# Optimization experiments

Hardware: AMD Instinct MI355X
Metric: run time of the kernel (lower is better)

## Reference

```python
import jax, jax.numpy as jnp
import numpy as np

B, T, C = 4, 2048, 1024
H = 16
D = C // H  # head_dim = 64


def setup_inputs() -> dict:
    key = jax.random.key(0)
    ks = jax.random.split(key, 9)
    s = 1.0 / np.sqrt(C)
    return {
        "x": jax.random.normal(ks[0], (B, T, C), dtype=jnp.float32),
        "Wq": jax.random.normal(ks[1], (C, C), dtype=jnp.float32) * s,
        "bq": jnp.zeros((C,), dtype=jnp.float32),
        "Wk": jax.random.normal(ks[2], (C, C), dtype=jnp.float32) * s,
        "bk": jnp.zeros((C,), dtype=jnp.float32),
        "Wv": jax.random.normal(ks[3], (C, C), dtype=jnp.float32) * s,
        "bv": jnp.zeros((C,), dtype=jnp.float32),
        "Wp": jax.random.normal(ks[4], (C, C), dtype=jnp.float32) * s,
        "bp": jnp.zeros((C,), dtype=jnp.float32),
    }


def reference(x, Wq, bq, Wk, bk, Wv, bv, Wp, bp):
    # Linear projections; reshape to [B, H, T, D]
    def split_heads(y):
        return y.reshape(B, T, H, D).transpose(0, 2, 1, 3)

    q = split_heads(x @ Wq + bq)
    k = split_heads(x @ Wk + bk)
    v = split_heads(x @ Wv + bv)

    scale = 1.0 / np.sqrt(D)
    att = jnp.einsum('bhqd,bhkd->bhqk', q, k) * scale  # [B,H,T,T]
    att = jax.nn.softmax(att, axis=-1)
    # dropout with p=0.0 is identity
    out = jnp.einsum('bhqk,bhkd->bhqd', att, v)        # [B,H,T,D]
    out = out.transpose(0, 2, 1, 3).reshape(B, T, C)
    return out @ Wp + bp
```

## Files before the change

kernel.cpp:

```cpp
#include <hip/hip_runtime.h>


#define B_ 4
#define T_ 2048
#define C_ 1024
#define H_ 16
#define D_ 64

#define QSCALE 0.18033688011112042f

typedef float  f32x4  __attribute__((ext_vector_type(4)));
typedef __bf16 bf16x8 __attribute__((ext_vector_type(8)));
typedef __bf16 bf16x4 __attribute__((ext_vector_type(4)));
typedef __bf16 bf16x2 __attribute__((ext_vector_type(2)));
typedef unsigned uint2v __attribute__((ext_vector_type(2)));

typedef const __attribute__((address_space(1))) void gv_t;
typedef __attribute__((address_space(3))) void lds_t;

__device__ __forceinline__ void async_load16(const void* g, void* l) {
  __builtin_amdgcn_global_load_lds((gv_t*)g, (lds_t*)l, 16, 0, 0);
}

__device__ __forceinline__ float fast_exp2(float x) {
#if __has_builtin(__builtin_amdgcn_exp2f)
  return __builtin_amdgcn_exp2f(x);
#else
  return exp2f(x);
#endif
}

__device__ __forceinline__ void pl16_swap(unsigned& a, unsigned& b) {
#if __has_builtin(__builtin_amdgcn_permlane16_swap)
  uint2v r = __builtin_amdgcn_permlane16_swap(a, b, false, false);
  a = r[0];
  b = r[1];
#else
  asm("v_permlane16_swap_b32 %0, %1" : "+v"(a), "+v"(b));
#endif
}

__global__ __launch_bounds__(256) void cast_f32_bf16(
    const float* __restrict__ in, __bf16* __restrict__ out, int n) {
  int i = (blockIdx.x * 256 + threadIdx.x) * 8;
  if (i >= n) return;
  float4 a = *(const float4*)(in + i);
  float4 b = *(const float4*)(in + i + 4);
  bf16x8 o;
  o[0] = (__bf16)a.x; o[1] = (__bf16)a.y; o[2] = (__bf16)a.z; o[3] = (__bf16)a.w;
  o[4] = (__bf16)b.x; o[5] = (__bf16)b.y; o[6] = (__bf16)b.z; o[7] = (__bf16)b.w;
  *(bf16x8*)(out + i) = o;
}

__global__ __launch_bounds__(256) void transpose_cast_w(
    const float* __restrict__ W0, const float* __restrict__ W1,
    const float* __restrict__ W2, const float* __restrict__ W3,
    __bf16* __restrict__ out) {
  int z = blockIdx.z;
  const float* W = (z == 0) ? W0 : (z == 1) ? W1 : (z == 2) ? W2 : W3;
  __bf16* o = out + (size_t)z * (C_ * C_);
  __shared__ __align__(16) __bf16 sT[64][72];
  int tid = threadIdx.x;
  int n0 = blockIdx.x * 64, k0 = blockIdx.y * 64;
#pragma unroll
  for (int i = 0; i < 4; i++) {
    int s = tid + i * 256;
    int kr = s >> 4, nc = (s & 15) * 4;
    float4 v = *(const float4*)&W[(size_t)(k0 + kr) * C_ + n0 + nc];
    bf16x4 t;
    t[0] = (__bf16)v.x; t[1] = (__bf16)v.y; t[2] = (__bf16)v.z; t[3] = (__bf16)v.w;
    *(bf16x4*)&sT[kr][nc] = t;
  }
  __syncthreads();
#pragma unroll
  for (int i = 0; i < 2; i++) {
    int s = tid + i * 256;
    int nr = s >> 3, kc = (s & 7) * 8;
    bf16x8 ov;
#pragma unroll
    for (int j = 0; j < 8; j++) ov[j] = sT[kc + j][nr];
    *(bf16x8*)&o[(size_t)(n0 + nr) * C_ + k0 + kc] = ov;
  }
}

template <typename OutT, int EPI>
__device__ __forceinline__ void gemm_body(
    const __bf16* __restrict__ A, const __bf16* __restrict__ Bt,
    const float* __restrict__ bias, OutT* __restrict__ C, int N, int K,
    float scale, int m0, int n0) {
  __shared__ __align__(16) __bf16 sA[128 * 32];
  __shared__ __align__(16) __bf16 sB[128 * 32];
  int tid = threadIdx.x, lane = tid & 63, wave = tid >> 6;
  int lr = lane & 15, quad = lane >> 4;
  int wm = (wave & 1) * 64, wn = (wave >> 1) * 64;

  const f32x4 zero = {0.f, 0.f, 0.f, 0.f};
  f32x4 acc[4][4];
#pragma unroll
  for (int i = 0; i < 4; i++)
#pragma unroll
    for (int j = 0; j < 4; j++) acc[i][j] = zero;

  for (int k0 = 0; k0 < K; k0 += 32) {
    __syncthreads();
#pragma unroll
    for (int i = 0; i < 2; i++) {
      int s = tid + i * 256;
      int r = s >> 2, c8 = (s & 3) * 8;
      async_load16(A + (size_t)(m0 + r) * K + k0 + c8, &sA[s * 8]);
      async_load16(Bt + (size_t)(n0 + r) * K + k0 + c8, &sB[s * 8]);
    }
    __syncthreads();
    bf16x8 af[4], bfr[4];
#pragma unroll
    for (int mt = 0; mt < 4; mt++)
      af[mt] = *(const bf16x8*)&sA[(wm + mt * 16 + lr) * 32 + quad * 8];
#pragma unroll
    for (int nt = 0; nt < 4; nt++)
      bfr[nt] = *(const bf16x8*)&sB[(wn + nt * 16 + lr) * 32 + quad * 8];
#pragma unroll
    for (int mt = 0; mt < 4; mt++)
#pragma unroll
      for (int nt = 0; nt < 4; nt++)
        acc[mt][nt] = __builtin_amdgcn_mfma_f32_16x16x32_bf16(
            af[mt], bfr[nt], acc[mt][nt], 0, 0, 0);
  }
  if (EPI == 0) {
#pragma unroll
    for (int mt = 0; mt < 4; mt++) {
#pragma unroll
      for (int nt = 0; nt < 4; nt++) {
        int n = n0 + wn + nt * 16 + lr;
        float bv = bias[n];
#pragma unroll
        for (int r = 0; r < 4; r++) {
          int m = m0 + wm + mt * 16 + quad * 4 + r;
          C[(size_t)m * N + n] = (OutT)((acc[mt][nt][r] + bv) * scale);
        }
      }
    }
  } else {
    int bb = m0 >> 11;
    int mloc0 = (m0 & (T_ - 1)) + wm;
    __bf16* Ct = (__bf16*)C;
#pragma unroll
    for (int mt = 0; mt < 4; mt++) {
      int pos = ((quad & 1) << 5) | ((((quad >> 1) << 1) | (mt & 1)) << 3) |
                ((mt >> 1) << 2);
#pragma unroll
      for (int nt = 0; nt < 4; nt++) {
        int n = n0 + wn + nt * 16 + lr;
        float bv = bias[n];
        bf16x4 ov;
#pragma unroll
        for (int r = 0; r < 4; r++) ov[r] = (__bf16)(acc[mt][nt][r] + bv);
        *(bf16x4*)&Ct[((size_t)bb * C_ + n) * T_ + mloc0 + pos] = ov;
      }
    }
  }
}

__global__ __launch_bounds__(256) void gemm_qkv_kernel(
    const __bf16* __restrict__ A, const __bf16* __restrict__ WT,
    const float* __restrict__ b0, const float* __restrict__ b1,
    const float* __restrict__ b2, __bf16* __restrict__ qkbase,
    __bf16* __restrict__ Vt) {
  int l = blockIdx.x;
  int xcd = l & 7;
  int idx = l >> 3;
  int z = idx >> 6;
  int rem = idx & 63;
  int m0 = (xcd * 8 + (rem >> 3)) * 128;
  int n0 = (rem & 7) * 128;
  if (z == 2) {
    gemm_body<__bf16, 1>(A, WT + (size_t)2 * C_ * C_, b2, Vt, C_, C_, 1.0f,
                         m0, n0);
  } else {
    const float* bias = (z == 0) ? b0 : b1;
    float scale = (z == 0) ? QSCALE : 1.0f;
    gemm_body<__bf16, 0>(A, WT + (size_t)z * C_ * C_, bias,
                         qkbase + (size_t)z * (B_ * T_) * C_, C_, C_, scale,
                         m0, n0);
  }
}

__global__ __launch_bounds__(256) void gemm_proj_kernel(
    const __bf16* __restrict__ A, const __bf16* __restrict__ Bt,
    const float* __restrict__ bias, float* __restrict__ C) {
  int l = blockIdx.x;
  int xcd = l & 7;
  int idx = l >> 3;
  int m0 = (xcd * 8 + (idx >> 3)) * 128;
  int n0 = (idx & 7) * 128;
  gemm_body<float, 0>(A, Bt, bias, C, C_, C_, 1.0f, m0, n0);
}

__global__ __launch_bounds__(256) void attn_kernel(
    const __bf16* __restrict__ Q, const __bf16* __restrict__ K,
    const __bf16* __restrict__ Vt, __bf16* __restrict__ O) {
  __shared__ __align__(16) __bf16 sK[64 * 72];
  __shared__ __align__(16) __bf16 sV[64 * 72];
  int tid = threadIdx.x, wave = tid >> 6, lane = tid & 63;
  int lr = lane & 15, quad = lane >> 4;
  int l = blockIdx.x;
  int bh = (l & 7) * 8 + ((l >> 3) & 7);
  int xbq = l >> 6;
  int b = bh >> 4, h = bh & 15;
  int qw = xbq * 256 + wave * 64;

  bf16x8 aq[4][2];
#pragma unroll
  for (int s = 0; s < 4; s++) {
    const __bf16* qp =
        Q + ((size_t)(b * T_ + qw + s * 16 + lr)) * C_ + h * D_ + quad * 8;
    aq[s][0] = *(const bf16x8*)qp;
    aq[s][1] = *(const bf16x8*)(qp + 32);
  }

  bf16x8 onesf;
#pragma unroll
  for (int j = 0; j < 8; j++) onesf[j] = (__bf16)1.0f;

  const f32x4 zero = {0.f, 0.f, 0.f, 0.f};
  f32x4 accO[4][4];
  f32x4 accL[4] = {zero, zero, zero, zero};
#pragma unroll
  for (int s = 0; s < 4; s++)
#pragma unroll
    for (int d = 0; d < 4; d++) accO[s][d] = zero;

  int srow[2], sc8[2];
#pragma unroll
  for (int i = 0; i < 2; i++) {
    int s = tid + i * 256;
    srow[i] = s >> 3;
    sc8[i] = (s & 7) * 8;
  }

  bf16x8 kreg[2], vreg[2];
#pragma unroll
  for (int i = 0; i < 2; i++) {
    kreg[i] = *(const bf16x8*)(K + ((size_t)(b * T_ + srow[i])) * C_ + h * D_ + sc8[i]);
    vreg[i] = *(const bf16x8*)(Vt + ((size_t)(bh * D_ + srow[i])) * T_ + sc8[i]);
  }

  for (int k0 = 0; k0 < T_; k0 += 64) {
    __builtin_amdgcn_sched_barrier(0);
    __builtin_amdgcn_s_barrier();
    __builtin_amdgcn_sched_barrier(0);
#pragma unroll
    for (int i = 0; i < 2; i++) {
      *(bf16x8*)&sK[srow[i] * 72 + sc8[i]] = kreg[i];
      *(bf16x8*)&sV[srow[i] * 72 + sc8[i]] = vreg[i];
    }
    __builtin_amdgcn_sched_barrier(0);
    asm volatile("s_waitcnt lgkmcnt(0)" ::: "memory");
    __builtin_amdgcn_s_barrier();
    __builtin_amdgcn_sched_barrier(0);

    if (k0 + 64 < T_) {
      int kn = k0 + 64;
#pragma unroll
      for (int i = 0; i < 2; i++) {
        kreg[i] = *(const bf16x8*)(K + ((size_t)(b * T_ + kn + srow[i])) * C_ + h * D_ + sc8[i]);
        vreg[i] = *(const bf16x8*)(Vt + ((size_t)(bh * D_ + srow[i])) * T_ + kn + sc8[i]);
      }
    }

    bf16x8 bkf[4][2];
#pragma unroll
    for (int nt = 0; nt < 4; nt++) {
      bkf[nt][0] = *(const bf16x8*)&sK[(nt * 16 + lr) * 72 + quad * 8];
      bkf[nt][1] = *(const bf16x8*)&sK[(nt * 16 + lr) * 72 + 32 + quad * 8];
    }

    bf16x8 bpA[4], bpB[4];
#pragma unroll
    for (int s = 0; s < 4; s++) {
      unsigned pw[4][2];
#pragma unroll
      for (int nt = 0; nt < 4; nt++) {
        f32x4 z = zero;
        z = __builtin_amdgcn_mfma_f32_16x16x32_bf16(bkf[nt][0], aq[s][0], z, 0, 0, 0);
        z = __builtin_amdgcn_mfma_f32_16x16x32_bf16(bkf[nt][1], aq[s][1], z, 0, 0, 0);
        union { bf16x2 h; unsigned u; } t0, t1;
        t0.h[0] = (__bf16)fast_exp2(z[0]);
        t0.h[1] = (__bf16)fast_exp2(z[1]);
        t1.h[0] = (__bf16)fast_exp2(z[2]);
        t1.h[1] = (__bf16)fast_exp2(z[3]);
        pw[nt][0] = t0.u;
        pw[nt][1] = t1.u;
      }
      unsigned a0 = pw[0][0], b0 = pw[1][0]; pl16_swap(a0, b0);
      unsigned a1 = pw[0][1], b1 = pw[1][1]; pl16_swap(a1, b1);
      unsigned a2 = pw[2][0], b2 = pw[3][0]; pl16_swap(a2, b2);
      unsigned a3 = pw[2][1], b3 = pw[3][1]; pl16_swap(a3, b3);
      union { unsigned u[4]; bf16x8 v; } pA, pB;
      pA.u[0] = a0; pA.u[1] = a1; pA.u[2] = a2; pA.u[3] = a3;
      pB.u[0] = b0; pB.u[1] = b1; pB.u[2] = b2; pB.u[3] = b3;
      bpA[s] = pA.v;
      bpB[s] = pB.v;
      accL[s] = __builtin_amdgcn_mfma_f32_16x16x32_bf16(onesf, bpA[s], accL[s], 0, 0, 0);
      accL[s] = __builtin_amdgcn_mfma_f32_16x16x32_bf16(onesf, bpB[s], accL[s], 0, 0, 0);
    }
#pragma unroll
    for (int dt = 0; dt < 4; dt++) {
      bf16x8 av0 = *(const bf16x8*)&sV[(dt * 16 + lr) * 72 + quad * 8];
      bf16x8 av1 = *(const bf16x8*)&sV[(dt * 16 + lr) * 72 + 32 + quad * 8];
#pragma unroll
      for (int s = 0; s < 4; s++) {
        accO[s][dt] = __builtin_amdgcn_mfma_f32_16x16x32_bf16(av0, bpA[s], accO[s][dt], 0, 0, 0);
        accO[s][dt] = __builtin_amdgcn_mfma_f32_16x16x32_bf16(av1, bpB[s], accO[s][dt], 0, 0, 0);
      }
    }
  }

#pragma unroll
  for (int s = 0; s < 4; s++) {
    float inv = 1.0f / accL[s][0];
    __bf16* op =
        O + ((size_t)(b * T_ + qw + s * 16 + lr)) * C_ + h * D_ + quad * 4;
#pragma unroll
    for (int dt = 0; dt < 4; dt++) {
      bf16x4 ov;
#pragma unroll
      for (int r = 0; r < 4; r++) ov[r] = (__bf16)(accO[s][dt][r] * inv);
      *(bf16x4*)&op[dt * 16] = ov;
    }
  }
}

extern "C" void kernel_launch(void* const* d_in, const int* in_sizes, int n_in,
                              void* d_out, int out_size, void* d_ws, size_t ws_size,
                              hipStream_t stream) {
  const float* x  = (const float*)d_in[0];
  const float* Wq = (const float*)d_in[1];
  const float* bq = (const float*)d_in[2];
  const float* Wk = (const float*)d_in[3];
  const float* bk = (const float*)d_in[4];
  const float* Wv = (const float*)d_in[5];
  const float* bv = (const float*)d_in[6];
  const float* Wp = (const float*)d_in[7];
  const float* bp = (const float*)d_in[8];
  float* out = (float*)d_out;

  char* ws = (char*)d_ws;
  const size_t MB = 1024 * 1024;
  __bf16* xb    = (__bf16*)(ws + 0 * MB);
  __bf16* WT    = (__bf16*)(ws + 16 * MB);
  __bf16* Qb    = (__bf16*)(ws + 24 * MB);
  __bf16* Kb    = Qb + (size_t)(B_ * T_) * C_;
  __bf16* Vt    = Kb + (size_t)(B_ * T_) * C_;
  __bf16* attnb = (__bf16*)(ws + 72 * MB);
  __bf16* WpT   = WT + (size_t)3 * C_ * C_;

  cast_f32_bf16<<<dim3(4096), dim3(256), 0, stream>>>(x, xb, B_ * T_ * C_);
  transpose_cast_w<<<dim3(16, 16, 4), dim3(256), 0, stream>>>(Wq, Wk, Wv, Wp, WT);
  gemm_qkv_kernel<<<dim3(1536), dim3(256), 0, stream>>>(xb, WT, bq, bk, bv, Qb, Vt);
  attn_kernel<<<dim3(512), dim3(256), 0, stream>>>(Qb, Kb, Vt, attnb);
  gemm_proj_kernel<<<dim3(512), dim3(256), 0, stream>>>(attnb, WpT, bp, out);
}
```

Baseline: 268.2 us.

## Merge prep kernels, halve proj GEMM N-tile, raise priority on PV MFMAs

Merges the x cast and the weight transpose-cast into one launch to save a kernel launch and overlap the two prep jobs. Templates the GEMM on the N tile width and runs the output projection with 128x64 tiles, doubling its grid to 1024 blocks so it fills the CUs better (256 CUs on MI355X). Adds s_setprio around the P·V MFMA block in attention to favour matrix issue across waves. The trade-off is more redundant A-tile loads in the projection GEMM.

New measurement: 267.5 us. Within noise of the previous version (-0.3%).

```diff
diff --git a/kernel.cpp b/kernel.cpp
--- a/kernel.cpp
+++ b/kernel.cpp
@@ -40,36 +40,38 @@
 #endif
 }
 
-__global__ __launch_bounds__(256) void cast_f32_bf16(
-    const float* __restrict__ in, __bf16* __restrict__ out, int n) {
-  int i = (blockIdx.x * 256 + threadIdx.x) * 8;
-  if (i >= n) return;
-  float4 a = *(const float4*)(in + i);
-  float4 b = *(const float4*)(in + i + 4);
-  bf16x8 o;
-  o[0] = (__bf16)a.x; o[1] = (__bf16)a.y; o[2] = (__bf16)a.z; o[3] = (__bf16)a.w;
-  o[4] = (__bf16)b.x; o[5] = (__bf16)b.y; o[6] = (__bf16)b.z; o[7] = (__bf16)b.w;
-  *(bf16x8*)(out + i) = o;
-}
-
-__global__ __launch_bounds__(256) void transpose_cast_w(
+__global__ __launch_bounds__(256) void prep_kernel(
+    const float* __restrict__ x, __bf16* __restrict__ xb,
     const float* __restrict__ W0, const float* __restrict__ W1,
     const float* __restrict__ W2, const float* __restrict__ W3,
-    __bf16* __restrict__ out) {
-  int z = blockIdx.z;
+    __bf16* __restrict__ wt) {
+  __shared__ __align__(16) __bf16 sT[64][72];
+  int l = blockIdx.x;
+  int tid = threadIdx.x;
+  if (l < 4096) {
+    int i = (l * 256 + tid) * 8;
+    float4 a = *(const float4*)(x + i);
+    float4 b = *(const float4*)(x + i + 4);
+    bf16x8 o;
+    o[0] = (__bf16)a.x; o[1] = (__bf16)a.y; o[2] = (__bf16)a.z; o[3] = (__bf16)a.w;
+    o[4] = (__bf16)b.x; o[5] = (__bf16)b.y; o[6] = (__bf16)b.z; o[7] = (__bf16)b.w;
+    *(bf16x8*)(xb + i) = o;
+    return;
+  }
+  int t = l - 4096;
+  int z = t >> 8;
+  int k0 = ((t >> 4) & 15) * 64;
+  int n0 = (t & 15) * 64;
   const float* W = (z == 0) ? W0 : (z == 1) ? W1 : (z == 2) ? W2 : W3;
-  __bf16* o = out + (size_t)z * (C_ * C_);
-  __shared__ __align__(16) __bf16 sT[64][72];
-  int tid = threadIdx.x;
-  int n0 = blockIdx.x * 64, k0 = blockIdx.y * 64;
+  __bf16* o = wt + (size_t)z * (C_ * C_);
 #pragma unroll
   for (int i = 0; i < 4; i++) {
     int s = tid + i * 256;
     int kr = s >> 4, nc = (s & 15) * 4;
     float4 v = *(const float4*)&W[(size_t)(k0 + kr) * C_ + n0 + nc];
-    bf16x4 t;
-    t[0] = (__bf16)v.x; t[1] = (__bf16)v.y; t[2] = (__bf16)v.z; t[3] = (__bf16)v.w;
-    *(bf16x4*)&sT[kr][nc] = t;
+    bf16x4 tt;
+    tt[0] = (__bf16)v.x; tt[1] = (__bf16)v.y; tt[2] = (__bf16)v.z; tt[3] = (__bf16)v.w;
+    *(bf16x4*)&sT[kr][nc] = tt;
   }
   __syncthreads();
 #pragma unroll
@@ -83,23 +85,25 @@
   }
 }
 
-template <typename OutT, int EPI>
+template <typename OutT, int EPI, int BN>
 __device__ __forceinline__ void gemm_body(
     const __bf16* __restrict__ A, const __bf16* __restrict__ Bt,
     const float* __restrict__ bias, OutT* __restrict__ C, int N, int K,
     float scale, int m0, int n0) {
   __shared__ __align__(16) __bf16 sA[128 * 32];
-  __shared__ __align__(16) __bf16 sB[128 * 32];
+  __shared__ __align__(16) __bf16 sB[BN * 32];
+  constexpr int NTW = BN / 32;
+  constexpr int NBU = BN * 4 / 256;
   int tid = threadIdx.x, lane = tid & 63, wave = tid >> 6;
   int lr = lane & 15, quad = lane >> 4;
-  int wm = (wave & 1) * 64, wn = (wave >> 1) * 64;
+  int wm = (wave & 1) * 64, wn = (wave >> 1) * (BN / 2);
 
   const f32x4 zero = {0.f, 0.f, 0.f, 0.f};
-  f32x4 acc[4][4];
+  f32x4 acc[4][NTW];
 #pragma unroll
   for (int i = 0; i < 4; i++)
 #pragma unroll
-    for (int j = 0; j < 4; j++) acc[i][j] = zero;
+    for (int j = 0; j < NTW; j++) acc[i][j] = zero;
 
   for (int k0 = 0; k0 < K; k0 += 32) {
     __syncthreads();
@@ -108,20 +112,25 @@
       int s = tid + i * 256;
       int r = s >> 2, c8 = (s & 3) * 8;
       async_load16(A + (size_t)(m0 + r) * K + k0 + c8, &sA[s * 8]);
+    }
+#pragma unroll
+    for (int i = 0; i < NBU; i++) {
+      int s = tid + i * 256;
+      int r = s >> 2, c8 = (s & 3) * 8;
       async_load16(Bt + (size_t)(n0 + r) * K + k0 + c8, &sB[s * 8]);
     }
     __syncthreads();
-    bf16x8 af[4], bfr[4];
+    bf16x8 af[4], bfr[NTW];
 #pragma unroll
     for (int mt = 0; mt < 4; mt++)
       af[mt] = *(const bf16x8*)&sA[(wm + mt * 16 + lr) * 32 + quad * 8];
 #pragma unroll
-    for (int nt = 0; nt < 4; nt++)
+    for (int nt = 0; nt < NTW; nt++)
       bfr[nt] = *(const bf16x8*)&sB[(wn + nt * 16 + lr) * 32 + quad * 8];
 #pragma unroll
     for (int mt = 0; mt < 4; mt++)
 #pragma unroll
-      for (int nt = 0; nt < 4; nt++)
+      for (int nt = 0; nt < NTW; nt++)
         acc[mt][nt] = __builtin_amdgcn_mfma_f32_16x16x32_bf16(
             af[mt], bfr[nt], acc[mt][nt], 0, 0, 0);
   }
@@ -129,7 +138,7 @@
 #pragma unroll
     for (int mt = 0; mt < 4; mt++) {
 #pragma unroll
-      for (int nt = 0; nt < 4; nt++) {
+      for (int nt = 0; nt < NTW; nt++) {
         int n = n0 + wn + nt * 16 + lr;
         float bv = bias[n];
 #pragma unroll
@@ -148,7 +157,7 @@
       int pos = ((quad & 1) << 5) | ((((quad >> 1) << 1) | (mt & 1)) << 3) |
                 ((mt >> 1) << 2);
 #pragma unroll
-      for (int nt = 0; nt < 4; nt++) {
+      for (int nt = 0; nt < NTW; nt++) {
         int n = n0 + wn + nt * 16 + lr;
         float bv = bias[n];
         bf16x4 ov;
@@ -173,14 +182,14 @@
   int m0 = (xcd * 8 + (rem >> 3)) * 128;
   int n0 = (rem & 7) * 128;
   if (z == 2) {
-    gemm_body<__bf16, 1>(A, WT + (size_t)2 * C_ * C_, b2, Vt, C_, C_, 1.0f,
-                         m0, n0);
+    gemm_body<__bf16, 1, 128>(A, WT + (size_t)2 * C_ * C_, b2, Vt, C_, C_,
+                              1.0f, m0, n0);
   } else {
     const float* bias = (z == 0) ? b0 : b1;
     float scale = (z == 0) ? QSCALE : 1.0f;
-    gemm_body<__bf16, 0>(A, WT + (size_t)z * C_ * C_, bias,
-                         qkbase + (size_t)z * (B_ * T_) * C_, C_, C_, scale,
-                         m0, n0);
+    gemm_body<__bf16, 0, 128>(A, WT + (size_t)z * C_ * C_, bias,
+                              qkbase + (size_t)z * (B_ * T_) * C_, C_, C_,
+                              scale, m0, n0);
   }
 }
 
@@ -190,9 +199,9 @@
   int l = blockIdx.x;
   int xcd = l & 7;
   int idx = l >> 3;
-  int m0 = (xcd * 8 + (idx >> 3)) * 128;
-  int n0 = (idx & 7) * 128;
-  gemm_body<float, 0>(A, Bt, bias, C, C_, C_, 1.0f, m0, n0);
+  int m0 = (xcd * 8 + (idx >> 4)) * 128;
+  int n0 = (idx & 15) * 64;
+  gemm_body<float, 0, 64>(A, Bt, bias, C, C_, C_, 1.0f, m0, n0);
 }
 
 __global__ __launch_bounds__(256) void attn_kernel(
@@ -283,11 +292,11 @@
         f32x4 z = zero;
         z = __builtin_amdgcn_mfma_f32_16x16x32_bf16(bkf[nt][0], aq[s][0], z, 0, 0, 0);
         z = __builtin_amdgcn_mfma_f32_16x16x32_bf16(bkf[nt][1], aq[s][1], z, 0, 0, 0);
-        union { bf16x2 h; unsigned u; } t0, t1;
-        t0.h[0] = (__bf16)fast_exp2(z[0]);
-        t0.h[1] = (__bf16)fast_exp2(z[1]);
-        t1.h[0] = (__bf16)fast_exp2(z[2]);
-        t1.h[1] = (__bf16)fast_exp2(z[3]);
+        union { bf16x2 h2; unsigned u; } t0, t1;
+        t0.h2[0] = (__bf16)fast_exp2(z[0]);
+        t0.h2[1] = (__bf16)fast_exp2(z[1]);
+        t1.h2[0] = (__bf16)fast_exp2(z[2]);
+        t1.h2[1] = (__bf16)fast_exp2(z[3]);
         pw[nt][0] = t0.u;
         pw[nt][1] = t1.u;
       }
@@ -303,6 +312,7 @@
       accL[s] = __builtin_amdgcn_mfma_f32_16x16x32_bf16(onesf, bpA[s], accL[s], 0, 0, 0);
       accL[s] = __builtin_amdgcn_mfma_f32_16x16x32_bf16(onesf, bpB[s], accL[s], 0, 0, 0);
     }
+    __builtin_amdgcn_s_setprio(1);
 #pragma unroll
     for (int dt = 0; dt < 4; dt++) {
       bf16x8 av0 = *(const bf16x8*)&sV[(dt * 16 + lr) * 72 + quad * 8];
@@ -313,6 +323,7 @@
         accO[s][dt] = __builtin_amdgcn_mfma_f32_16x16x32_bf16(av1, bpB[s], accO[s][dt], 0, 0, 0);
       }
     }
+    __builtin_amdgcn_s_setprio(0);
   }
 
 #pragma unroll
@@ -354,9 +365,8 @@
   __bf16* attnb = (__bf16*)(ws + 72 * MB);
   __bf16* WpT   = WT + (size_t)3 * C_ * C_;
 
-  cast_f32_bf16<<<dim3(4096), dim3(256), 0, stream>>>(x, xb, B_ * T_ * C_);
-  transpose_cast_w<<<dim3(16, 16, 4), dim3(256), 0, stream>>>(Wq, Wk, Wv, Wp, WT);
+  prep_kernel<<<dim3(5120), dim3(256), 0, stream>>>(x, xb, Wq, Wk, Wv, Wp, WT);
   gemm_qkv_kernel<<<dim3(1536), dim3(256), 0, stream>>>(xb, WT, bq, bk, bv, Qb, Vt);
   attn_kernel<<<dim3(512), dim3(256), 0, stream>>>(Qb, Kb, Vt, attnb);
-  gemm_proj_kernel<<<dim3(512), dim3(256), 0, stream>>>(attnb, WpT, bp, out);
-}
+  gemm_proj_kernel<<<dim3(1024), dim3(256), 0, stream>>>(attnb, WpT, bp, out);
+}
```
